# Performance work log

Hardware: AMD Instinct MI355X
Metric: run time of the kernel (lower is better)

Reference implementation:

```python
import jax, jax.numpy as jnp
import numpy as np

ALPHA = 0.2  # LeakyReLU slope in GAT
OUT_SLOPE = 0.01  # default nn.LeakyyReLU slope for self.out
B, E, IN_DIM, HID, HEADS = 4, 2048, 32, 18, 3
DH = HID // HEADS  # per-head out dim = 6


def _leaky(x, slope):
    return jnp.where(x > 0, x, slope * x)


def _gat_head(x, adj, W, a):
    # x: [B,E,in], W: [in,dh], a: [2*dh,1]
    h = jnp.einsum('bei,id->bed', x, W)                      # [B,E,dh]
    d = h.shape[-1]
    # score[b,i,j] = leakyrelu(a . concat(h_i, h_j)) = leakyrelu(h_i.a1 + h_j.a2)
    e1 = jnp.einsum('bed,d->be', h, a[:d, 0])
    e2 = jnp.einsum('bed,d->be', h, a[d:, 0])
    score = _leaky(e1[:, :, None] + e2[:, None, :], ALPHA)   # [B,E,E]
    scores = jnp.where(adj == 1.0, score, 0.0)
    logits = jnp.where(adj > 0.0, scores, -30.0)
    att = jax.nn.softmax(logits, axis=2)                     # softmax over j
    # h_prime[b,j,d] = sum_i att[b,i,j] * h[b,i,d]  (torch sums over dim=1)
    h_prime = jnp.einsum('bij,bid->bjd', att, h)
    return jax.nn.elu(h_prime)  # concat=True -> elu


def _gat_multihead(x, adj, Ws, As):
    # Ws: [H,in,dh], As: [H,2*dh,1]
    outs = jax.vmap(lambda W, a: _gat_head(x, adj, W, a))(Ws, As)  # [H,B,E,dh]
    H, b, e, d = outs.shape
    return jnp.moveaxis(outs, 0, 2).reshape(b, e, H * d)  # concat heads last-dim


def _gcn(x, adj2d, W, b):
    return adj2d @ (x @ W) + b


def setup_inputs() -> dict:
    key = jax.random.key(0)
    ks = jax.random.split(key, 16)
    node_input = jax.random.normal(ks[0], (B, E, IN_DIM), jnp.float32)
    uv_filed = jax.random.normal(ks[1], (B, E, IN_DIM), jnp.float32)
    adj = jax.random.randint(ks[2], (B, E, E), 0, 2).astype(jnp.float32)
    s = 0.1
    Wt1 = jax.random.normal(ks[3], (HEADS, IN_DIM, DH), jnp.float32) * s
    at1 = jax.random.normal(ks[4], (HEADS, 2 * DH, 1), jnp.float32) * s
    Wt2 = jax.random.normal(ks[5], (HEADS, IN_DIM, DH), jnp.float32) * s
    at2 = jax.random.normal(ks[6], (HEADS, 2 * DH, 1), jnp.float32) * s
    Wg1 = jax.random.normal(ks[7], (HID, 16), jnp.float32) * s
    bg1 = jnp.zeros((16,), jnp.float32)
    Wg2 = jax.random.normal(ks[8], (16, 2), jnp.float32) * s
    bg2 = jnp.zeros((2,), jnp.float32)
    Wo1 = jax.random.normal(ks[9], (HID, 16), jnp.float32) * s
    bo1 = jnp.zeros((16,), jnp.float32)
    Wo2 = jax.random.normal(ks[10], (16, 2), jnp.float32) * s
    bo2 = jnp.zeros((2,), jnp.float32)
    return dict(node_input=node_input, uv_filed=uv_filed, adj=adj,
                Wt1=Wt1, at1=at1, Wt2=Wt2, at2=at2,
                Wg1=Wg1, bg1=bg1, Wg2=Wg2, bg2=bg2,
                Wo1=Wo1, bo1=bo1, Wo2=Wo2, bo2=bo2)


def reference(node_input, uv_filed, adj, Wt1, at1, Wt2, at2,
              Wg1, bg1, Wg2, bg2, Wo1, bo1, Wo2, bo2):
    h = _gat_multihead(node_input, adj, Wt1, at1)  # [B,E,18]
    o = _gat_multihead(uv_filed, adj, Wt2, at2)    # [B,E,18]
    a0 = adj[0]
    Y = jax.nn.relu(_gcn(h[0], a0, Wg1, bg1))
    O = jax.nn.relu(_gcn(o[0], a0, Wo1, bo1))
    Y = _gcn(Y, a0, Wg2, bg2)
    O = _gcn(O, a0, Wo2, bo2)
    return (jax.nn.log_softmax(Y, axis=1), _leaky(O, OUT_SLOPE))
```

## Files before the change

### kernel.cpp

```cpp
#include <hip/hip_runtime.h>
#include <hip/hip_bf16.h>


__global__ __launch_bounds__(256) void k1_features(
    const float* __restrict__ node, const float* __restrict__ uv,
    const float* __restrict__ Wt1, const float* __restrict__ at1,
    const float* __restrict__ Wt2, const float* __restrict__ at2,
    float* __restrict__ hcol, float* __restrict__ pack1, float* __restrict__ pack2) {
  __shared__ float sW[192];
  __shared__ float sA[12];
  int b = blockIdx.x;
  int g = b / 24;
  int h = (b / 8) % 3;
  int e = (b % 8) * 256 + threadIdx.x;
  const float* W = (g ? Wt2 : Wt1) + h * 192;
  const float* A = (g ? at2 : at1) + h * 12;
  const float* x = (g ? uv : node) + e * 32;
  if (threadIdx.x < 192) sW[threadIdx.x] = W[threadIdx.x];
  if (threadIdx.x < 12) sA[threadIdx.x] = A[threadIdx.x];
  __syncthreads();
  float xv[32];
#pragma unroll
  for (int i = 0; i < 32; ++i) xv[i] = x[i];
  float hv[6];
#pragma unroll
  for (int d = 0; d < 6; ++d) hv[d] = 0.f;
#pragma unroll
  for (int i = 0; i < 32; ++i)
#pragma unroll
    for (int d = 0; d < 6; ++d) hv[d] += xv[i] * sW[i * 6 + d];
  float e1 = 0.f, e2 = 0.f;
#pragma unroll
  for (int d = 0; d < 6; ++d) {
    e1 += hv[d] * sA[d];
    e2 += hv[d] * sA[6 + d];
  }
  int c = g * 3 + h;
#pragma unroll
  for (int d = 0; d < 6; ++d) hcol[(c * 6 + d) * 2048 + e] = hv[d];
  pack1[c * 2048 + e] = e1;
  pack1[(6 + c) * 2048 + e] = __expf(e1);
  pack1[(12 + c) * 2048 + e] = __expf(0.2f * e1);
  pack2[c * 2048 + e] = e2;
  pack2[(6 + c) * 2048 + e] = __expf(e2);
  pack2[(12 + c) * 2048 + e] = __expf(0.2f * e2);
}

__global__ __launch_bounds__(384) void k2_rowsum(
    const float* __restrict__ adj0, const float* __restrict__ pack1,
    const float* __restrict__ pack2, float* __restrict__ invrs) {
  int tid = threadIdx.x;
  int c = tid >> 6, lane = tid & 63;
  int i0 = blockIdx.x * 4;
  const float4* adj4 = (const float4*)adj0;
  const float4* p2_4 = (const float4*)pack2;
  float e1r[4], p1r[4], q1r[4], sum[4];
#pragma unroll
  for (int r = 0; r < 4; ++r) {
    e1r[r] = pack1[c * 2048 + i0 + r];
    p1r[r] = pack1[(6 + c) * 2048 + i0 + r];
    q1r[r] = pack1[(12 + c) * 2048 + i0 + r];
    sum[r] = 0.f;
  }
#pragma unroll
  for (int it = 0; it < 8; ++it) {
    int j4 = it * 64 + lane;
    float4 e2 = p2_4[c * 512 + j4];
    float4 p2 = p2_4[(6 + c) * 512 + j4];
    float4 q2 = p2_4[(12 + c) * 512 + j4];
    float4 av[4];
#pragma unroll
    for (int r = 0; r < 4; ++r) av[r] = adj4[(i0 + r) * 512 + j4];
#pragma unroll
    for (int r = 0; r < 4; ++r) {
      float s0, s1, s2, s3;
      { float e = e1r[r] + e2.x; bool p = e > 0.f;
        s0 = av[r].x * (p ? p1r[r] : q1r[r]) * (p ? p2.x : q2.x); }
      { float e = e1r[r] + e2.y; bool p = e > 0.f;
        s1 = av[r].y * (p ? p1r[r] : q1r[r]) * (p ? p2.y : q2.y); }
      { float e = e1r[r] + e2.z; bool p = e > 0.f;
        s2 = av[r].z * (p ? p1r[r] : q1r[r]) * (p ? p2.z : q2.z); }
      { float e = e1r[r] + e2.w; bool p = e > 0.f;
        s3 = av[r].w * (p ? p1r[r] : q1r[r]) * (p ? p2.w : q2.w); }
      sum[r] += (s0 + s1) + (s2 + s3);
    }
  }
#pragma unroll
  for (int r = 0; r < 4; ++r) {
#pragma unroll
    for (int off = 32; off > 0; off >>= 1) sum[r] += __shfl_down(sum[r], off);
  }
  if (lane == 0) {
#pragma unroll
    for (int r = 0; r < 4; ++r) invrs[c * 2048 + i0 + r] = 1.0f / sum[r];
  }
}

__global__ __launch_bounds__(384) void k3_hprime(
    const float* __restrict__ adj0, const float* __restrict__ hcol,
    const float* __restrict__ pack1, const float* __restrict__ pack2,
    const float* __restrict__ invrs, float* __restrict__ hp) {
  __shared__ float sAdj[64 * 64];
  __shared__ float4 sPack[6 * 64];
  __shared__ float sHS[6 * 64 * 8];
  float4* sAdj4 = (float4*)sAdj;
  const float4* adj4 = (const float4*)adj0;
  float4* sHS4 = (float4*)sHS;
  int tid = threadIdx.x;
  int c6 = tid >> 6, jl = tid & 63;
  int j0 = blockIdx.x * 64;
  int j = j0 + jl;
  float e2v = pack2[c6 * 2048 + j];
  float p2v = pack2[(6 + c6) * 2048 + j];
  float q2v = pack2[(12 + c6) * 2048 + j];
  float acc0 = 0.f, acc1 = 0.f, acc2 = 0.f, acc3 = 0.f, acc4 = 0.f, acc5 = 0.f;
  int ibeg = blockIdx.y * 128, iend = ibeg + 128;
  for (int i0 = ibeg; i0 < iend; i0 += 64) {
    __syncthreads();
    for (int idx = tid; idx < 1024; idx += 384) {
      int ii = idx >> 4, c4 = idx & 15;
      sAdj4[ii * 16 + c4] = adj4[(i0 + ii) * 512 + (j0 >> 2) + c4];
    }
    {
      int cc = c6, ii = jl;
      float e1 = pack1[cc * 2048 + i0 + ii];
      float p1 = pack1[(6 + cc) * 2048 + i0 + ii];
      float q1 = pack1[(12 + cc) * 2048 + i0 + ii];
      sPack[cc * 64 + ii] = make_float4(e1, p1, q1, 0.f);
      float iv = invrs[cc * 2048 + i0 + ii];
#pragma unroll
      for (int d = 0; d < 6; ++d)
        sHS[(cc * 64 + ii) * 8 + d] = hcol[(cc * 6 + d) * 2048 + i0 + ii] * iv;
      sHS[(cc * 64 + ii) * 8 + 6] = 0.f;
      sHS[(cc * 64 + ii) * 8 + 7] = 0.f;
    }
    __syncthreads();
#pragma unroll 8
    for (int ii = 0; ii < 64; ++ii) {
      float adjv = sAdj[ii * 64 + jl];
      float4 pk = sPack[c6 * 64 + ii];
      float4 h0 = sHS4[(c6 * 64 + ii) * 2];
      float4 h1 = sHS4[(c6 * 64 + ii) * 2 + 1];
      float e = pk.x + e2v;
      bool pos = e > 0.f;
      float w = adjv * (pos ? pk.y : pk.z) * (pos ? p2v : q2v);
      acc0 += w * h0.x;
      acc1 += w * h0.y;
      acc2 += w * h0.z;
      acc3 += w * h0.w;
      acc4 += w * h1.x;
      acc5 += w * h1.y;
    }
  }
  int kb = c6 * 6;
  atomicAdd(&hp[(kb + 0) * 2048 + j], acc0);
  atomicAdd(&hp[(kb + 1) * 2048 + j], acc1);
  atomicAdd(&hp[(kb + 2) * 2048 + j], acc2);
  atomicAdd(&hp[(kb + 3) * 2048 + j], acc3);
  atomicAdd(&hp[(kb + 4) * 2048 + j], acc4);
  atomicAdd(&hp[(kb + 5) * 2048 + j], acc5);
}

__global__ __launch_bounds__(256) void k4_T(
    const float* __restrict__ hp, const float* __restrict__ Wg1,
    const float* __restrict__ Wo1, float* __restrict__ T) {
  __shared__ float sHP[32 * 37];
  __shared__ float sWg[288], sWo[288];
  int tid = threadIdx.x;
  int j0 = blockIdx.x * 32;
  for (int idx = tid; idx < 288; idx += 256) {
    sWg[idx] = Wg1[idx];
    sWo[idx] = Wo1[idx];
  }
  for (int idx = tid; idx < 1152; idx += 256) {
    int r = idx >> 5, jl = idx & 31;
    sHP[jl * 37 + r] = hp[r * 2048 + j0 + jl];
  }
  __syncthreads();
  int jl = tid & 31, wq = tid >> 5;
  int gat = wq >> 2;
  int c0 = (wq & 3) * 4;
  const float* Wp = gat ? sWo : sWg;
  float acc[4];
#pragma unroll
  for (int t = 0; t < 4; ++t) acc[t] = 0.f;
#pragma unroll
  for (int r = 0; r < 18; ++r) {
    float x = sHP[jl * 37 + gat * 18 + r];
    float hc = x > 0.f ? x : __expf(x) - 1.f;
#pragma unroll
    for (int t = 0; t < 4; ++t) acc[t] += hc * Wp[r * 16 + c0 + t];
  }
#pragma unroll
  for (int t = 0; t < 4; ++t) T[(j0 + jl) * 32 + gat * 16 + c0 + t] = acc[t];
}

__global__ __launch_bounds__(256) void k5_gcn1(
    const float* __restrict__ adj0, const float* __restrict__ T,
    float* __restrict__ Craw) {
  __shared__ float sAtT[64 * 33];
  __shared__ float sT[64 * 32];
  float4* sT4 = (float4*)sT;
  const float4* adj4 = (const float4*)adj0;
  const float4* T4 = (const float4*)T;
  int tid = threadIdx.x;
  int row = tid & 31, cg = tid >> 5;
  int i0 = blockIdx.x * 32;
  int k0 = blockIdx.y * 128;
  float acc0 = 0.f, acc1 = 0.f, acc2 = 0.f, acc3 = 0.f;
  for (int kb = k0; kb < k0 + 128; kb += 64) {
    __syncthreads();
    for (int idx = tid; idx < 512; idx += 256) {
      int r = idx >> 4, kq = idx & 15;
      float4 a = adj4[(i0 + r) * 512 + (kb >> 2) + kq];
      sAtT[(kq * 4 + 0) * 33 + r] = a.x;
      sAtT[(kq * 4 + 1) * 33 + r] = a.y;
      sAtT[(kq * 4 + 2) * 33 + r] = a.z;
      sAtT[(kq * 4 + 3) * 33 + r] = a.w;
    }
    for (int idx = tid; idx < 512; idx += 256) sT4[idx] = T4[kb * 8 + idx];
    __syncthreads();
#pragma unroll 16
    for (int k = 0; k < 64; ++k) {
      float a = sAtT[k * 33 + row];
      float4 t = sT4[k * 8 + cg];
      acc0 += a * t.x;
      acc1 += a * t.y;
      acc2 += a * t.z;
      acc3 += a * t.w;
    }
  }
  float* dst = &Craw[(i0 + row) * 32 + cg * 4];
  atomicAdd(dst + 0, acc0);
  atomicAdd(dst + 1, acc1);
  atomicAdd(dst + 2, acc2);
  atomicAdd(dst + 3, acc3);
}

__global__ __launch_bounds__(256) void k6_T2(
    const float* __restrict__ Craw, const float* __restrict__ bg1,
    const float* __restrict__ Wg2, const float* __restrict__ bo1,
    const float* __restrict__ Wo2, float* __restrict__ T2) {
  int tid = threadIdx.x;
  int wave = tid >> 6, lane = tid & 63;
  int j = blockIdx.x * 8 + wave * 2 + (lane >> 5);
  int cl = lane & 31;
  int gat = cl >> 4, cc = cl & 15;
  float x = Craw[j * 32 + cl];
  x += gat ? bo1[cc] : bg1[cc];
  x = x > 0.f ? x : 0.f;
  float wa = gat ? Wo2[cc * 2 + 0] : Wg2[cc * 2 + 0];
  float wb = gat ? Wo2[cc * 2 + 1] : Wg2[cc * 2 + 1];
  float pa = x * wa, pb = x * wb;
#pragma unroll
  for (int m = 8; m > 0; m >>= 1) {
    pa += __shfl_xor(pa, m);
    pb += __shfl_xor(pb, m);
  }
  if (cc == 0) {
    T2[j * 4 + gat * 2 + 0] = pa;
    T2[j * 4 + gat * 2 + 1] = pb;
  }
}

__global__ __launch_bounds__(256) void k7_final(
    const float* __restrict__ adj0, const float* __restrict__ T2,
    const float* __restrict__ bg2, const float* __restrict__ bo2,
    float* __restrict__ out) {
  int tid = threadIdx.x;
  int lane = tid & 63, w = tid >> 6;
  int r = blockIdx.x * 4 + w;
  const float4* adj4 = (const float4*)adj0;
  const float4* T24 = (const float4*)T2;
  float4 acc = make_float4(0.f, 0.f, 0.f, 0.f);
#pragma unroll
  for (int it = 0; it < 8; ++it) {
    int k4 = it * 64 + lane;
    float4 av = adj4[r * 512 + k4];
    float4 t0 = T24[k4 * 4 + 0];
    float4 t1 = T24[k4 * 4 + 1];
    float4 t2 = T24[k4 * 4 + 2];
    float4 t3 = T24[k4 * 4 + 3];
    acc.x += av.x * t0.x + av.y * t1.x + av.z * t2.x + av.w * t3.x;
    acc.y += av.x * t0.y + av.y * t1.y + av.z * t2.y + av.w * t3.y;
    acc.z += av.x * t0.z + av.y * t1.z + av.z * t2.z + av.w * t3.z;
    acc.w += av.x * t0.w + av.y * t1.w + av.z * t2.w + av.w * t3.w;
  }
#pragma unroll
  for (int off = 32; off > 0; off >>= 1) {
    acc.x += __shfl_down(acc.x, off);
    acc.y += __shfl_down(acc.y, off);
    acc.z += __shfl_down(acc.z, off);
    acc.w += __shfl_down(acc.w, off);
  }
  if (lane == 0) {
    float y0 = acc.x + bg2[0], y1 = acc.y + bg2[1];
    float m = fmaxf(y0, y1);
    float ls = m + logf(__expf(y0 - m) + __expf(y1 - m));
    out[r * 2 + 0] = y0 - ls;
    out[r * 2 + 1] = y1 - ls;
    float o0 = acc.z + bo2[0], o1 = acc.w + bo2[1];
    out[4096 + r * 2 + 0] = o0 > 0.f ? o0 : 0.01f * o0;
    out[4096 + r * 2 + 1] = o1 > 0.f ? o1 : 0.01f * o1;
  }
}

extern "C" void kernel_launch(void* const* d_in, const int* in_sizes, int n_in,
                              void* d_out, int out_size, void* d_ws, size_t ws_size,
                              hipStream_t stream) {
  const float* node = (const float*)d_in[0];
  const float* uv = (const float*)d_in[1];
  const float* adj = (const float*)d_in[2];
  const float* Wt1 = (const float*)d_in[3];
  const float* at1 = (const float*)d_in[4];
  const float* Wt2 = (const float*)d_in[5];
  const float* at2 = (const float*)d_in[6];
  const float* Wg1 = (const float*)d_in[7];
  const float* bg1 = (const float*)d_in[8];
  const float* Wg2 = (const float*)d_in[9];
  const float* bg2 = (const float*)d_in[10];
  const float* Wo1 = (const float*)d_in[11];
  const float* bo1 = (const float*)d_in[12];
  const float* Wo2 = (const float*)d_in[13];
  const float* bo2 = (const float*)d_in[14];
  float* ws = (float*)d_ws;
  float* hcol = ws;
  float* pack1 = ws + 73728;
  float* pack2 = ws + 110592;
  float* invrs = ws + 147456;
  float* T = ws + 159744;
  float* T2 = ws + 225280;
  float* hp = ws + 233472;
  float* Craw = ws + 307200;
  float* out = (float*)d_out;

  hipMemsetAsync(hp, 0, (73728 + 65536) * sizeof(float), stream);
  k1_features<<<48, 256, 0, stream>>>(node, uv, Wt1, at1, Wt2, at2, hcol, pack1, pack2);
  k2_rowsum<<<512, 384, 0, stream>>>(adj, pack1, pack2, invrs);
  k3_hprime<<<dim3(32, 16), 384, 0, stream>>>(adj, hcol, pack1, pack2, invrs, hp);
  k4_T<<<64, 256, 0, stream>>>(hp, Wg1, Wo1, T);
  k5_gcn1<<<dim3(64, 16), 256, 0, stream>>>(adj, T, Craw);
  k6_T2<<<256, 256, 0, stream>>>(Craw, bg1, Wg2, bo1, Wo2, T2);
  k7_final<<<512, 256, 0, stream>>>(adj, T2, bg2, bo2, out);
}
```

Measured before the change: 208.7 us.

## Replace shared-memory tiled GCN1 matmul with direct per-thread global-load dot products

The first GCN aggregation kernel no longer stages adjacency and T tiles in LDS with a transpose and barriers. Each thread now computes one output element over a 512-long K slice, reading adjacency and T directly from global memory. The grid changes to 256x4 blocks, which also cuts the number of atomic adds per output. The cost is lost data reuse: the adjacency loads are broadcast within each half-wave but not coalesced across k, so performance depends on cache hits and K-loop latency.

```diff
diff --git a/kernel.cpp b/kernel.cpp
--- a/kernel.cpp
+++ b/kernel.cpp
@@ -198,43 +198,19 @@
 __global__ __launch_bounds__(256) void k5_gcn1(
     const float* __restrict__ adj0, const float* __restrict__ T,
     float* __restrict__ Craw) {
-  __shared__ float sAtT[64 * 33];
-  __shared__ float sT[64 * 32];
-  float4* sT4 = (float4*)sT;
-  const float4* adj4 = (const float4*)adj0;
-  const float4* T4 = (const float4*)T;
-  int tid = threadIdx.x;
-  int row = tid & 31, cg = tid >> 5;
-  int i0 = blockIdx.x * 32;
-  int k0 = blockIdx.y * 128;
-  float acc0 = 0.f, acc1 = 0.f, acc2 = 0.f, acc3 = 0.f;
-  for (int kb = k0; kb < k0 + 128; kb += 64) {
-    __syncthreads();
-    for (int idx = tid; idx < 512; idx += 256) {
-      int r = idx >> 4, kq = idx & 15;
-      float4 a = adj4[(i0 + r) * 512 + (kb >> 2) + kq];
-      sAtT[(kq * 4 + 0) * 33 + r] = a.x;
-      sAtT[(kq * 4 + 1) * 33 + r] = a.y;
-      sAtT[(kq * 4 + 2) * 33 + r] = a.z;
-      sAtT[(kq * 4 + 3) * 33 + r] = a.w;
-    }
-    for (int idx = tid; idx < 512; idx += 256) sT4[idx] = T4[kb * 8 + idx];
-    __syncthreads();
+  int tid = threadIdx.x;
+  int lane = tid & 63, w = tid >> 6;
+  int c = lane & 31, rh = lane >> 5;
+  int r = blockIdx.x * 8 + w * 2 + rh;
+  int k0 = blockIdx.y * 512;
+  const float* arow = adj0 + (size_t)r * 2048 + k0;
+  const float* tcol = T + (size_t)k0 * 32 + c;
+  float acc = 0.f;
 #pragma unroll 16
-    for (int k = 0; k < 64; ++k) {
-      float a = sAtT[k * 33 + row];
-      float4 t = sT4[k * 8 + cg];
-      acc0 += a * t.x;
-      acc1 += a * t.y;
-      acc2 += a * t.z;
-      acc3 += a * t.w;
-    }
-  }
-  float* dst = &Craw[(i0 + row) * 32 + cg * 4];
-  atomicAdd(dst + 0, acc0);
-  atomicAdd(dst + 1, acc1);
-  atomicAdd(dst + 2, acc2);
-  atomicAdd(dst + 3, acc3);
+  for (int k = 0; k < 512; ++k) {
+    acc += arow[k] * tcol[k * 32];
+  }
+  atomicAdd(&Craw[r * 32 + c], acc);
 }
 
 __global__ __launch_bounds__(256) void k6_T2(
@@ -339,7 +315,7 @@
   k2_rowsum<<<512, 384, 0, stream>>>(adj, pack1, pack2, invrs);
   k3_hprime<<<dim3(32, 16), 384, 0, stream>>>(adj, hcol, pack1, pack2, invrs, hp);
   k4_T<<<64, 256, 0, stream>>>(hp, Wg1, Wo1, T);
-  k5_gcn1<<<dim3(64, 16), 256, 0, stream>>>(adj, T, Craw);
+  k5_gcn1<<<dim3(256, 4), 256, 0, stream>>>(adj, T, Craw);
   k6_T2<<<256, 256, 0, stream>>>(Craw, bg1, Wg2, bo1, Wo2, T2);
   k7_final<<<512, 256, 0, stream>>>(adj, T2, bg2, bo2, out);
 }
```

Measured after the change: 196.6 us. 1.06x faster.
